# Kernel tuning notes

Measured on AMD Instinct MI355X. Metric: run time of the kernel, lower is better.

The kernel has to match this reference:

```python
import jax, jax.numpy as jnp
import numpy as np

B, S, E, H = 2, 2048, 1024, 16
HD = E // H  # 64
NEG = -1e24


def setup_inputs() -> dict:
    key = jax.random.key(0)
    ks = jax.random.split(key, 20)
    sc_e = 1.0 / np.sqrt(E)
    inp = {
        "q_matrix": jax.random.normal(ks[0], (B, S, E), jnp.float32),
        "k_matrix": jax.random.normal(ks[1], (B, S, E), jnp.float32),
        "v_matrix": jax.random.normal(ks[2], (B, S, E), jnp.float32),
        "mask": jax.random.randint(ks[3], (B, S, S), 0, 2).astype(bool),
        # global QKV projections (embed_dim -> embed_dim)
        "Wq": jax.random.normal(ks[4], (E, E), jnp.float32) * sc_e,
        "bq": jnp.zeros((E,), jnp.float32),
        "Wk": jax.random.normal(ks[5], (E, E), jnp.float32) * sc_e,
        "bk": jnp.zeros((E,), jnp.float32),
        "Wv": jax.random.normal(ks[6], (E, E), jnp.float32) * sc_e,
        "bv": jnp.zeros((E,), jnp.float32),
        # per-head QKV projections (embed_dim -> head_dim), batched over heads
        "Whq": jax.random.normal(ks[7], (H, E, HD), jnp.float32) * sc_e,
        "bhq": jnp.zeros((H, HD), jnp.float32),
        "Whk": jax.random.normal(ks[8], (H, E, HD), jnp.float32) * sc_e,
        "bhk": jnp.zeros((H, HD), jnp.float32),
        "Whv": jax.random.normal(ks[9], (H, E, HD), jnp.float32) * sc_e,
        "bhv": jnp.zeros((H, HD), jnp.float32),
        # output projection
        "Wo": jax.random.normal(ks[10], (E, E), jnp.float32) * sc_e,
        "bo": jnp.zeros((E,), jnp.float32),
    }
    return inp


def reference(q_matrix, k_matrix, v_matrix, mask, Wq, bq, Wk, bk, Wv, bv,
              Whq, bhq, Whk, bhk, Whv, bhv, Wo, bo):
    # global projections [B,S,E]
    qg = q_matrix @ Wq + bq
    kg = k_matrix @ Wk + bk
    vg = v_matrix @ Wv + bv
    # per-head projections -> [B,H,S,HD]
    qh = jnp.einsum('bse,hed->bhsd', qg, Whq) + bhq[None, :, None, :]
    kh = jnp.einsum('bse,hed->bhsd', kg, Whk) + bhk[None, :, None, :]
    vh = jnp.einsum('bse,hed->bhsd', vg, Whv) + bhv[None, :, None, :]
    # scaled dot-product attention, scores [B,H,S,S]
    scores = jnp.einsum('bhsd,bhtd->bhst', qh, kh) / jnp.sqrt(jnp.float32(HD))
    scores = jnp.where(mask[:, None, :, :], NEG, scores)
    weights = jax.nn.softmax(scores, axis=-1)
    out = jnp.einsum('bhst,bhtd->bhsd', weights, vh)
    # concat heads (head order along last dim, matching torch.cat)
    x = out.transpose(0, 2, 1, 3).reshape(out.shape[0], out.shape[2], E)
    return x @ Wo + bo
```

## Files before the change

### kernel.cpp

```cpp
#include <hip/hip_runtime.h>
#include <hip/hip_bf16.h>

typedef unsigned short us16;
typedef __attribute__((ext_vector_type(8))) short short8;
typedef __attribute__((ext_vector_type(4))) float float4v;

#define E_DIM 1024
#define S_LEN 2048
#define B_DIM 2
#define H_DIM 16
#define HD_DIM 64
#define M_ROWS 4096
#define SCALE2 0.18033688011112042f

__device__ __forceinline__ float b2f(us16 b) {
    return __uint_as_float(((unsigned int)b) << 16);
}
__device__ __forceinline__ us16 f2b(float f) {
    unsigned int u = __float_as_uint(f);
    unsigned int r = (u + 0x7fffu + ((u >> 16) & 1u)) >> 16;
    return (us16)r;
}
__device__ __forceinline__ unsigned pack2(float a, float b) {
    return ((__float_as_uint(a) + 0x8000u) >> 16) |
           ((__float_as_uint(b) + 0x8000u) & 0xFFFF0000u);
}

__device__ __forceinline__ void gload16(const us16* g, us16* lds_uniform_base) {
    __builtin_amdgcn_global_load_lds(
        (const __attribute__((address_space(1))) void*)g,
        (__attribute__((address_space(3))) void*)lds_uniform_base, 16, 0, 0);
}

__global__ __launch_bounds__(256) void prep(
    const float* __restrict__ q, const float* __restrict__ k, const float* __restrict__ v,
    const float* __restrict__ Wq, const float* __restrict__ Wk, const float* __restrict__ Wv,
    const float* __restrict__ Whq, const float* __restrict__ Whk, const float* __restrict__ Whv,
    const float* __restrict__ Wo,
    const float* __restrict__ bq, const float* __restrict__ bk, const float* __restrict__ bv,
    const float* __restrict__ bhq, const float* __restrict__ bhk, const float* __restrict__ bhv,
    const int* __restrict__ mask,
    us16* qb, us16* kb, us16* vb, us16* Wqb, us16* Wkb, us16* Wvb,
    us16* WhqT, us16* WhkT, us16* WhvT, us16* WoT,
    unsigned long long* mbits,
    float* bcq, float* bck, float* bcv, float* zbias)
{
    __shared__ us16 tile[32][33];
    __shared__ float red[4][64];
    int blk = blockIdx.x, tid = threadIdx.x;

    if (blk < 7680) {
        const float* in; us16* out; int idx;
        if (blk < 6144) {
            int z = blk >> 11, rem = blk & 2047;
            in = z == 0 ? q : z == 1 ? k : v;
            out = z == 0 ? qb : z == 1 ? kb : vb;
            idx = (rem * 256 + tid) * 8;
        } else {
            int t = blk - 6144, z = t >> 9, rem = t & 511;
            in = z == 0 ? Wq : z == 1 ? Wk : Wv;
            out = z == 0 ? Wqb : z == 1 ? Wkb : Wvb;
            idx = (rem * 256 + tid) * 8;
        }
        float4 f0 = *(const float4*)(in + idx);
        float4 f1 = *(const float4*)(in + idx + 4);
        us16 t8[8] = {f2b(f0.x), f2b(f0.y), f2b(f0.z), f2b(f0.w),
                      f2b(f1.x), f2b(f1.y), f2b(f1.z), f2b(f1.w)};
        *(uint4*)(out + idx) = *(const uint4*)t8;
    } else if (blk < 11776) {
        int t = blk - 7680, z = t >> 10, rem = t & 1023;
        const float* in = z == 0 ? Whq : z == 1 ? Whk : z == 2 ? Whv : Wo;
        us16* out = z == 0 ? WhqT : z == 1 ? WhkT : z == 2 ? WhvT : WoT;
        int mode = (z < 3) ? 1 : 0;
        int bx = rem & 31, by = rem >> 5;
        int tx = tid & 31, ty = tid >> 5;
#pragma unroll
        for (int i = 0; i < 4; ++i) {
            int e = by * 32 + ty + i * 8;
            int c = bx * 32 + tx;
            size_t src;
            if (mode == 0) src = (size_t)e * E_DIM + c;
            else           src = ((size_t)(c >> 6) * E_DIM + e) * 64 + (c & 63);
            tile[ty + i * 8][tx] = f2b(in[src]);
        }
        __syncthreads();
#pragma unroll
        for (int i = 0; i < 4; ++i) {
            int c = bx * 32 + ty + i * 8;
            int e = by * 32 + tx;
            out[(size_t)c * E_DIM + e] = tile[tx][ty + i * 8];
        }
    } else if (blk < 12800) {
        int row = (blk - 11776) * 4 + (tid >> 6);
        int lane = tid & 63;
        const int* mp = mask + (size_t)row * S_LEN;
        for (int w = 0; w < 32; ++w) {
            int mv = mp[w * 64 + lane];
            unsigned long long bal = __ballot(mv != 0);
            if (lane == 0) mbits[(size_t)row * 32 + w] = bal;
        }
    } else if (blk < 12848) {
        int t = blk - 12800, z = t >> 4, h = t & 15;
        const float* bg = z == 0 ? bq : z == 1 ? bk : bv;
        const float* Wh = z == 0 ? Whq : z == 1 ? Whk : Whv;
        const float* bh = z == 0 ? bhq : z == 1 ? bhk : bhv;
        float* bc = z == 0 ? bcq : z == 1 ? bck : bcv;
        float sc = (z == 0) ? SCALE2 : 1.0f;
        int d = tid & 63, part = tid >> 6;
        float acc = 0.f;
        int j0 = part * 256;
        for (int j = j0; j < j0 + 256; ++j)
            acc += bg[j] * Wh[((size_t)h * E_DIM + j) * HD_DIM + d];
        red[part][d] = acc;
        __syncthreads();
        if (tid < 64)
            bc[h * 64 + tid] = (red[0][tid] + red[1][tid] + red[2][tid] + red[3][tid] + bh[h * 64 + tid]) * sc;
    } else {
        int i = (blk - 12848) * 256 + tid;
        if (i < 1024) zbias[i] = 0.f;
    }
}

#define BK 32

__device__ __forceinline__ void gemm_body(
    const us16* __restrict__ A, const us16* __restrict__ Bt,
    const float* __restrict__ bias, void* __restrict__ Cp,
    int M, int N, int K, int bxt, int byt, int omode)
{
    __shared__ us16 As[128 * BK];
    __shared__ us16 Bs[128 * BK];

    int tid = threadIdx.x;
    int wave = tid >> 6, lane = tid & 63;
    int quad = lane >> 4, l16 = lane & 15;
    int wm = (wave >> 1) * 64, wn = (wave & 1) * 64;
    int bm0 = byt * 128, bn0 = bxt * 128;
    int srow = lane >> 2;
    int gcol = (((lane & 3) ^ (srow & 3)) << 3);
    int rslot = ((quad ^ (l16 & 3)) << 3);

    float4v acc[4][4];
#pragma unroll
    for (int i = 0; i < 4; ++i)
#pragma unroll
        for (int j = 0; j < 4; ++j)
#pragma unroll
            for (int r = 0; r < 4; ++r) acc[i][j][r] = 0.f;

    for (int k0 = 0; k0 < K; k0 += BK) {
#pragma unroll
        for (int c = 0; c < 2; ++c) {
            int r0 = 32 * wave + 16 * c;
            gload16(A  + (size_t)(bm0 + r0 + srow) * K + k0 + gcol, &As[r0 * BK]);
            gload16(Bt + (size_t)(bn0 + r0 + srow) * K + k0 + gcol, &Bs[r0 * BK]);
        }
        __syncthreads();
        short8 af[4], bfr[4];
#pragma unroll
        for (int i = 0; i < 4; ++i)
            af[i] = *(const short8*)&As[(wm + i * 16 + l16) * BK + rslot];
#pragma unroll
        for (int j = 0; j < 4; ++j)
            bfr[j] = *(const short8*)&Bs[(wn + j * 16 + l16) * BK + rslot];
#pragma unroll
        for (int i = 0; i < 4; ++i)
#pragma unroll
            for (int j = 0; j < 4; ++j)
                acc[i][j] = __builtin_amdgcn_mfma_f32_16x16x32_bf16(af[i], bfr[j], acc[i][j], 0, 0, 0);
        __syncthreads();
    }

#pragma unroll
    for (int i = 0; i < 4; ++i) {
#pragma unroll
        for (int j = 0; j < 4; ++j) {
#pragma unroll
            for (int r = 0; r < 4; ++r) {
                int row = bm0 + wm + i * 16 + quad * 4 + r;
                int col = bn0 + wn + j * 16 + l16;
                float vv = acc[i][j][r] + ((omode == 3) ? bias[row] : bias[col]);
                if (omode == 1) {
                    int b = row >> 11, s = row & 2047, h = col >> 6, d = col & 63;
                    ((us16*)Cp)[(((size_t)(b * H_DIM + h) * S_LEN + s) * HD_DIM) + d] = f2b(vv);
                } else {
                    int h = row >> 6, d = row & 63, b = col >> 11, sl = col & 2047;
                    ((us16*)Cp)[(((size_t)(b * H_DIM + h) * HD_DIM + d) * S_LEN) + sl] = f2b(vv);
                }
            }
        }
    }
}

__global__ __launch_bounds__(256) void proj_all(
    const us16* __restrict__ qb, const us16* __restrict__ kb, const us16* __restrict__ vb,
    const us16* __restrict__ WcqT, const us16* __restrict__ WckT, const us16* __restrict__ WcvT,
    const float* __restrict__ bcq, const float* __restrict__ bck, const float* __restrict__ bcv,
    us16* __restrict__ qhb, us16* __restrict__ khb, us16* __restrict__ vtb)
{
    int bx = blockIdx.x;
    int z = bx >> 8, t = bx & 255;
    if (z == 0)      gemm_body(qb, WcqT, bcq, qhb, M_ROWS, E_DIM, E_DIM, t & 7, t >> 3, 1);
    else if (z == 1) gemm_body(kb, WckT, bck, khb, M_ROWS, E_DIM, E_DIM, t & 7, t >> 3, 1);
    else             gemm_body(WcvT, vb, bcv, vtb, E_DIM, M_ROWS, E_DIM, t & 31, t >> 5, 3);
}

template<int OMODE>
__device__ __forceinline__ void gemm64_body(
    const us16* __restrict__ A, const us16* __restrict__ Bt,
    const float* __restrict__ bias, void* __restrict__ Cp,
    int M, int N, int K, int bxt, int byt, float oscale)
{
    __shared__ us16 As[64 * BK];
    __shared__ us16 Bs[128 * BK];

    int tid = threadIdx.x;
    int wave = tid >> 6, lane = tid & 63;
    int quad = lane >> 4, l16 = lane & 15;
    int wm = (wave >> 1) * 32, wn = (wave & 1) * 64;
    int bm0 = byt * 64, bn0 = bxt * 128;
    int srow = lane >> 2;
    int gcol = (((lane & 3) ^ (srow & 3)) << 3);
    int rslot = ((quad ^ (l16 & 3)) << 3);

    float4v acc[2][4];
#pragma unroll
    for (int i = 0; i < 2; ++i)
#pragma unroll
        for (int j = 0; j < 4; ++j)
#pragma unroll
            for (int r = 0; r < 4; ++r) acc[i][j][r] = 0.f;

    for (int k0 = 0; k0 < K; k0 += BK) {
        gload16(A + (size_t)(bm0 + 16 * wave + srow) * K + k0 + gcol, &As[16 * wave * BK]);
#pragma unroll
        for (int c = 0; c < 2; ++c) {
            int r0 = 32 * wave + 16 * c;
            gload16(Bt + (size_t)(bn0 + r0 + srow) * K + k0 + gcol, &Bs[r0 * BK]);
        }
        __syncthreads();
        short8 af[2], bfr[4];
#pragma unroll
        for (int i = 0; i < 2; ++i)
            af[i] = *(const short8*)&As[(wm + i * 16 + l16) * BK + rslot];
#pragma unroll
        for (int j = 0; j < 4; ++j)
            bfr[j] = *(const short8*)&Bs[(wn + j * 16 + l16) * BK + rslot];
#pragma unroll
        for (int i = 0; i < 2; ++i)
#pragma unroll
            for (int j = 0; j < 4; ++j)
                acc[i][j] = __builtin_amdgcn_mfma_f32_16x16x32_bf16(af[i], bfr[j], acc[i][j], 0, 0, 0);
        __syncthreads();
    }

#pragma unroll
    for (int i = 0; i < 2; ++i)
#pragma unroll
        for (int j = 0; j < 4; ++j)
#pragma unroll
            for (int r = 0; r < 4; ++r) {
                int row = bm0 + wm + i * 16 + quad * 4 + r;
                int col = bn0 + wn + j * 16 + l16;
                float vv = (acc[i][j][r] + bias[col]) * oscale;
                if (OMODE == 0) ((us16*)Cp)[(size_t)row * N + col] = f2b(vv);
                else            ((float*)Cp)[(size_t)row * N + col] = vv;
            }
}

__global__ __launch_bounds__(256) void wgemm3(
    const us16* A0, const us16* A1, const us16* A2,
    const us16* B0, const us16* B1, const us16* B2,
    const float* zbias, us16* C0, us16* C1, us16* C2)
{
    int z = blockIdx.z;
    const us16* A = z == 0 ? A0 : z == 1 ? A1 : A2;
    const us16* Bt = z == 0 ? B0 : z == 1 ? B1 : B2;
    us16* C = z == 0 ? C0 : z == 1 ? C1 : C2;
    float sc = (z == 0) ? SCALE2 : 1.0f;
    gemm64_body<0>(A, Bt, zbias, C, E_DIM, E_DIM, E_DIM, blockIdx.x, blockIdx.y, sc);
}

__global__ __launch_bounds__(256) void gemm_out64(
    const us16* __restrict__ A, const us16* __restrict__ Bt,
    const float* __restrict__ bias, float* __restrict__ C, int M, int N, int K)
{
    gemm64_body<2>(A, Bt, bias, C, M, N, K, blockIdx.x, blockIdx.y, 1.0f);
}

#define PST 72
#define NT 16

__global__ __launch_bounds__(512) void attn_kernel(
    const us16* __restrict__ qh, const us16* __restrict__ kh,
    const us16* __restrict__ vt, const unsigned long long* __restrict__ mbits,
    us16* __restrict__ o_p, float* __restrict__ l_p)
{
    __shared__ us16 Ks[2][64 * 64];
    __shared__ us16 Vs[2][64 * 64];
    __shared__ us16 Pw[8][16 * PST];

    int tid = threadIdx.x;
    int w = tid >> 6, lane = tid & 63;
    int quad = lane >> 4, l16 = lane & 15;

    int wg = blockIdx.x;
    int xcd = wg & 7, idx = wg >> 3;
    int bh = xcd * 4 + (idx >> 5);
    int rem = idx & 31;
    int z = rem >> 4;
    int q0 = (rem & 15) * 128;
    int b = bh >> 4;
    const size_t base = (size_t)bh * (S_LEN * HD_DIM);

    int qrow = q0 + w * 16 + l16;
    short8 qf0, qf1;
    {
        const us16* qp = qh + base + (size_t)qrow * HD_DIM + quad * 8;
        qf0 = *(const short8*)qp;
        qf1 = *(const short8*)(qp + 32);
    }

    int strow = w * 8 + (lane >> 3);
    int scol = ((lane & 7) ^ (strow & 7)) * 8;
    const us16* ksrc0 = kh + base + ((size_t)(z * 1024 + strow)) * HD_DIM + scol;
    const us16* vsrc0 = vt + base + (size_t)strow * S_LEN + scol + z * 1024;

    int slotA = (quad ^ (l16 & 7)) * 8;
    int slotB = slotA ^ 32;

    float lsum = 0.f;
    float4v o[4];
#pragma unroll
    for (int dt = 0; dt < 4; ++dt)
#pragma unroll
        for (int r = 0; r < 4; ++r) o[dt][r] = 0.f;

    const unsigned long long* mrow = mbits + ((size_t)(b * S_LEN + qrow) * 32) + z * 16;

    gload16(ksrc0, &Ks[0][w * 512]);
    gload16(vsrc0, &Vs[0][w * 512]);
    unsigned long long mw = mrow[0];
    asm volatile("s_waitcnt vmcnt(0)" ::: "memory");
    __builtin_amdgcn_s_barrier();
    __builtin_amdgcn_sched_barrier(0);

    for (int t = 0; t < NT; ++t) {
        int cur = t & 1;
        const us16* KsC = Ks[cur];
        const us16* VsC = Vs[cur];

        unsigned long long mwn = 0ull;
        if (t + 1 < NT) {
            gload16(ksrc0 + (size_t)((t + 1) * 64) * HD_DIM, &Ks[cur ^ 1][w * 512]);
            gload16(vsrc0 + (t + 1) * 64, &Vs[cur ^ 1][w * 512]);
            mwn = mrow[t + 1];
        }

        float4v sc[4];
        __builtin_amdgcn_s_setprio(1);
#pragma unroll
        for (int ct = 0; ct < 4; ++ct) {
            int tt = ct * 16 + l16;
            short8 kf0 = *(const short8*)&KsC[tt * 64 + slotA];
            short8 kf1 = *(const short8*)&KsC[tt * 64 + slotB];
            float4v a;
#pragma unroll
            for (int r = 0; r < 4; ++r) a[r] = 0.f;
            a = __builtin_amdgcn_mfma_f32_16x16x32_bf16(kf0, qf0, a, 0, 0, 0);
            a = __builtin_amdgcn_mfma_f32_16x16x32_bf16(kf1, qf1, a, 0, 0, 0);
            sc[ct] = a;
        }
        __builtin_amdgcn_s_setprio(0);

#pragma unroll
        for (int ct = 0; ct < 4; ++ct) {
            unsigned bits = (unsigned)(mw >> (ct * 16 + quad * 4));
            float p[4];
#pragma unroll
            for (int r = 0; r < 4; ++r) {
                float pin = ((bits >> r) & 1u) ? -1e38f : sc[ct][r];
                p[r] = __builtin_amdgcn_exp2f(pin);
                lsum += p[r];
            }
            uint2 pk;
            pk.x = pack2(p[0], p[1]);
            pk.y = pack2(p[2], p[3]);
            *(uint2*)&Pw[w][l16 * PST + ct * 16 + quad * 4] = pk;
        }

        short8 pf0 = *(const short8*)&Pw[w][l16 * PST + quad * 8];
        short8 pf1 = *(const short8*)&Pw[w][l16 * PST + 32 + quad * 8];
        __builtin_amdgcn_s_setprio(1);
#pragma unroll
        for (int dt = 0; dt < 4; ++dt) {
            int d = dt * 16 + l16;
            short8 vf0 = *(const short8*)&VsC[d * 64 + slotA];
            short8 vf1 = *(const short8*)&VsC[d * 64 + slotB];
            o[dt] = __builtin_amdgcn_mfma_f32_16x16x32_bf16(pf0, vf0, o[dt], 0, 0, 0);
            o[dt] = __builtin_amdgcn_mfma_f32_16x16x32_bf16(pf1, vf1, o[dt], 0, 0, 0);
        }
        __builtin_amdgcn_s_setprio(0);

        mw = mwn;
        asm volatile("s_waitcnt vmcnt(0)" ::: "memory");
        __builtin_amdgcn_s_barrier();
        __builtin_amdgcn_sched_barrier(0);
    }

    lsum += __shfl_xor(lsum, 16, 64);
    lsum += __shfl_xor(lsum, 32, 64);
    if (lane < 16)
        l_p[(size_t)z * 65536 + bh * S_LEN + qrow] = lsum;

    int rowg = bh * S_LEN + q0 + w * 16 + quad * 4;
#pragma unroll
    for (int dt = 0; dt < 4; ++dt)
#pragma unroll
        for (int r = 0; r < 4; ++r)
            o_p[(size_t)z * 4194304 + (size_t)(rowg + r) * 64 + dt * 16 + l16] = f2b(o[dt][r]);
}

__global__ __launch_bounds__(256) void attn_combine(
    const us16* __restrict__ o_p, const float* __restrict__ l_p,
    us16* __restrict__ x)
{
    int fidx = blockIdx.x * 256 + threadIdx.x;
    int rix = fidx >> 3;
    int d8 = (fidx & 7) * 8;
    float linv = 1.0f / (l_p[rix] + l_p[65536 + rix]);
    uint4 a = *(const uint4*)(o_p + (size_t)rix * 64 + d8);
    uint4 c = *(const uint4*)(o_p + 4194304 + (size_t)rix * 64 + d8);
    const us16* ap = (const us16*)&a;
    const us16* cp = (const us16*)&c;
    us16 t8[8];
#pragma unroll
    for (int i = 0; i < 8; ++i)
        t8[i] = f2b((b2f(ap[i]) + b2f(cp[i])) * linv);
    int bh = rix >> 11, b = bh >> 4, h = bh & 15, s = rix & 2047;
    *(uint4*)&x[(size_t)(b * S_LEN + s) * E_DIM + h * HD_DIM + d8] = *(const uint4*)t8;
}

extern "C" void kernel_launch(void* const* d_in, const int* in_sizes, int n_in,
                              void* d_out, int out_size, void* d_ws, size_t ws_size,
                              hipStream_t stream) {
    const float* q    = (const float*)d_in[0];
    const float* k    = (const float*)d_in[1];
    const float* v    = (const float*)d_in[2];
    const int*   mask = (const int*)d_in[3];
    const float* Wq = (const float*)d_in[4];   const float* bq = (const float*)d_in[5];
    const float* Wk = (const float*)d_in[6];   const float* bk = (const float*)d_in[7];
    const float* Wv = (const float*)d_in[8];   const float* bv = (const float*)d_in[9];
    const float* Whq = (const float*)d_in[10]; const float* bhq = (const float*)d_in[11];
    const float* Whk = (const float*)d_in[12]; const float* bhk = (const float*)d_in[13];
    const float* Whv = (const float*)d_in[14]; const float* bhv = (const float*)d_in[15];
    const float* Wo = (const float*)d_in[16];  const float* bo = (const float*)d_in[17];

    us16* ws = (us16*)d_ws;
    const size_t M1 = (size_t)1 << 20;
    us16* WhqT = ws + 0 * M1;
    us16* WhkT = ws + 1 * M1;
    us16* WhvT = ws + 2 * M1;
    us16* WoT  = ws + 3 * M1;
    us16* WcqT = ws + 4 * M1;
    us16* WckT = ws + 5 * M1;
    us16* WcvT = ws + 6 * M1;
    us16* Wqb  = ws + 7 * M1;
    us16* Wkb  = ws + 8 * M1;
    us16* Wvb  = ws + 9 * M1;
    us16* qb   = ws + 10 * M1;
    us16* kb   = ws + 14 * M1;
    us16* vb   = ws + 18 * M1;
    us16* qhb  = ws + 22 * M1;
    us16* khb  = ws + 26 * M1;
    us16* vtb  = ws + 30 * M1;
    us16* o_p  = qb;
    us16* xb   = vb;
    float* bcq   = (float*)(ws + 34 * M1);
    float* bck   = bcq + 1024;
    float* bcv   = bck + 1024;
    float* zbias = bcv + 1024;
    unsigned long long* mbits = (unsigned long long*)(ws + 34 * M1 + 16384);
    float* l_p = (float*)(ws + 34 * M1 + 16384 + 524288);

    prep<<<12852, 256, 0, stream>>>(q, k, v, Wq, Wk, Wv, Whq, Whk, Whv, Wo,
                                    bq, bk, bv, bhq, bhk, bhv, mask,
                                    qb, kb, vb, Wqb, Wkb, Wvb,
                                    WhqT, WhkT, WhvT, WoT, mbits,
                                    bcq, bck, bcv, zbias);

    wgemm3<<<dim3(8, 16, 3), 256, 0, stream>>>(WhqT, WhkT, WhvT, Wqb, Wkb, Wvb, zbias,
                                               WcqT, WckT, WcvT);

    proj_all<<<768, 256, 0, stream>>>(qb, kb, vb, WcqT, WckT, WcvT,
                                      bcq, bck, bcv, qhb, khb, vtb);

    attn_kernel<<<1024, 512, 0, stream>>>(qhb, khb, vtb, mbits, o_p, l_p);
    attn_combine<<<2048, 256, 0, stream>>>(o_p, l_p, xb);

    gemm_out64<<<dim3(8, 64), 256, 0, stream>>>(xb, WoT, bo, (float*)d_out,
                                                M_ROWS, E_DIM, E_DIM);
}
```

Measured before the change: 319.9 us.

## Fold mask into MFMA accumulator init and compute row sums via ones-MFMA

```diff
diff --git a/kernel.cpp b/kernel.cpp
--- a/kernel.cpp
+++ b/kernel.cpp
@@ -20,10 +20,6 @@
     unsigned int u = __float_as_uint(f);
     unsigned int r = (u + 0x7fffu + ((u >> 16) & 1u)) >> 16;
     return (us16)r;
-}
-__device__ __forceinline__ unsigned pack2(float a, float b) {
-    return ((__float_as_uint(a) + 0x8000u) >> 16) |
-           ((__float_as_uint(b) + 0x8000u) & 0xFFFF0000u);
 }
 
 __device__ __forceinline__ void gload16(const us16* g, us16* lds_uniform_base) {
@@ -42,7 +38,7 @@
     const int* __restrict__ mask,
     us16* qb, us16* kb, us16* vb, us16* Wqb, us16* Wkb, us16* Wvb,
     us16* WhqT, us16* WhkT, us16* WhvT, us16* WoT,
-    unsigned long long* mbits,
+    us16* marr,
     float* bcq, float* bck, float* bcv, float* zbias)
 {
     __shared__ us16 tile[32][33];
@@ -90,17 +86,25 @@
             int e = by * 32 + tx;
             out[(size_t)c * E_DIM + e] = tile[tx][ty + i * 8];
         }
-    } else if (blk < 12800) {
-        int row = (blk - 11776) * 4 + (tid >> 6);
-        int lane = tid & 63;
-        const int* mp = mask + (size_t)row * S_LEN;
-        for (int w = 0; w < 32; ++w) {
-            int mv = mp[w * 64 + lane];
-            unsigned long long bal = __ballot(mv != 0);
-            if (lane == 0) mbits[(size_t)row * 32 + w] = bal;
-        }
-    } else if (blk < 12848) {
-        int t = blk - 12800, z = t >> 4, h = t & 15;
+    } else if (blk < 15872) {
+        int g = (blk - 11776) * 256 + tid;
+        int lane = g & 63, ld = (g >> 6) & 1, wv = (g >> 7) & 7;
+        int q0t = (g >> 10) & 15, ktz = (g >> 14) & 31, bb = g >> 19;
+        int quad = lane >> 4, l16 = lane & 15;
+        int qq = q0t * 128 + wv * 16 + l16;
+        int t0 = ktz * 64 + ld * 32 + quad * 4;
+        const int* mp = mask + ((size_t)bb * S_LEN + qq) * S_LEN + t0;
+        int4 ma = *(const int4*)mp;
+        int4 mb2 = *(const int4*)(mp + 16);
+        const us16 NEGB = f2b(-1e38f);
+        us16 t8[8];
+        t8[0] = ma.x ? NEGB : (us16)0;  t8[1] = ma.y ? NEGB : (us16)0;
+        t8[2] = ma.z ? NEGB : (us16)0;  t8[3] = ma.w ? NEGB : (us16)0;
+        t8[4] = mb2.x ? NEGB : (us16)0; t8[5] = mb2.y ? NEGB : (us16)0;
+        t8[6] = mb2.z ? NEGB : (us16)0; t8[7] = mb2.w ? NEGB : (us16)0;
+        *(uint4*)&marr[(size_t)g * 8] = *(const uint4*)t8;
+    } else if (blk < 15920) {
+        int t = blk - 15872, z = t >> 4, h = t & 15;
         const float* bg = z == 0 ? bq : z == 1 ? bk : bv;
         const float* Wh = z == 0 ? Whq : z == 1 ? Whk : Whv;
         const float* bh = z == 0 ? bhq : z == 1 ? bhk : bhv;
@@ -116,7 +120,7 @@
         if (tid < 64)
             bc[h * 64 + tid] = (red[0][tid] + red[1][tid] + red[2][tid] + red[3][tid] + bh[h * 64 + tid]) * sc;
     } else {
-        int i = (blk - 12848) * 256 + tid;
+        int i = (blk - 15920) * 256 + tid;
         if (i < 1024) zbias[i] = 0.f;
     }
 }
@@ -293,7 +297,7 @@
 
 __global__ __launch_bounds__(512) void attn_kernel(
     const us16* __restrict__ qh, const us16* __restrict__ kh,
-    const us16* __restrict__ vt, const unsigned long long* __restrict__ mbits,
+    const us16* __restrict__ vt, const us16* __restrict__ marr,
     us16* __restrict__ o_p, float* __restrict__ l_p)
 {
     __shared__ us16 Ks[2][64 * 64];
@@ -309,7 +313,8 @@
     int bh = xcd * 4 + (idx >> 5);
     int rem = idx & 31;
     int z = rem >> 4;
-    int q0 = (rem & 15) * 128;
+    int q0t = rem & 15;
+    int q0 = q0t * 128;
     int b = bh >> 4;
     const size_t base = (size_t)bh * (S_LEN * HD_DIM);
 
@@ -321,26 +326,34 @@
         qf1 = *(const short8*)(qp + 32);
     }
 
+    short8 onesf;
+#pragma unroll
+    for (int j = 0; j < 8; ++j) onesf[j] = (short)0x3F80;
+
     int strow = w * 8 + (lane >> 3);
     int scol = ((lane & 7) ^ (strow & 7)) * 8;
     const us16* ksrc0 = kh + base + ((size_t)(z * 1024 + strow)) * HD_DIM + scol;
     const us16* vsrc0 = vt + base + (size_t)strow * S_LEN + scol + z * 1024;
 
+    const us16* mb0p = marr + ((((size_t)(b * 32 + z * 16) * 16 + q0t) * 8 + w) * 1024)
+                            + (size_t)lane * 8;
+
     int slotA = (quad ^ (l16 & 7)) * 8;
     int slotB = slotA ^ 32;
 
-    float lsum = 0.f;
     float4v o[4];
 #pragma unroll
     for (int dt = 0; dt < 4; ++dt)
 #pragma unroll
         for (int r = 0; r < 4; ++r) o[dt][r] = 0.f;
-
-    const unsigned long long* mrow = mbits + ((size_t)(b * S_LEN + qrow) * 32) + z * 16;
+    float4v o_l;
+#pragma unroll
+    for (int r = 0; r < 4; ++r) o_l[r] = 0.f;
 
     gload16(ksrc0, &Ks[0][w * 512]);
     gload16(vsrc0, &Vs[0][w * 512]);
-    unsigned long long mw = mrow[0];
+    uint4 mc0 = *(const uint4*)(mb0p);
+    uint4 mc1 = *(const uint4*)(mb0p + 512);
     asm volatile("s_waitcnt vmcnt(0)" ::: "memory");
     __builtin_amdgcn_s_barrier();
     __builtin_amdgcn_sched_barrier(0);
@@ -350,11 +363,13 @@
         const us16* KsC = Ks[cur];
         const us16* VsC = Vs[cur];
 
-        unsigned long long mwn = 0ull;
+        uint4 mn0 = mc0, mn1 = mc1;
         if (t + 1 < NT) {
             gload16(ksrc0 + (size_t)((t + 1) * 64) * HD_DIM, &Ks[cur ^ 1][w * 512]);
             gload16(vsrc0 + (t + 1) * 64, &Vs[cur ^ 1][w * 512]);
-            mwn = mrow[t + 1];
+            const us16* mp = mb0p + (size_t)(t + 1) * 131072;
+            mn0 = *(const uint4*)(mp);
+            mn1 = *(const uint4*)(mp + 512);
         }
 
         float4v sc[4];
@@ -364,9 +379,16 @@
             int tt = ct * 16 + l16;
             short8 kf0 = *(const short8*)&KsC[tt * 64 + slotA];
             short8 kf1 = *(const short8*)&KsC[tt * 64 + slotB];
+            unsigned w0, w1;
+            if (ct == 0)      { w0 = mc0.x; w1 = mc0.y; }
+            else if (ct == 1) { w0 = mc0.z; w1 = mc0.w; }
+            else if (ct == 2) { w0 = mc1.x; w1 = mc1.y; }
+            else              { w0 = mc1.z; w1 = mc1.w; }
             float4v a;
-#pragma unroll
-            for (int r = 0; r < 4; ++r) a[r] = 0.f;
+            a[0] = __uint_as_float(w0 << 16);
+            a[1] = __uint_as_float(w0 & 0xFFFF0000u);
+            a[2] = __uint_as_float(w1 << 16);
+            a[3] = __uint_as_float(w1 & 0xFFFF0000u);
             a = __builtin_amdgcn_mfma_f32_16x16x32_bf16(kf0, qf0, a, 0, 0, 0);
             a = __builtin_amdgcn_mfma_f32_16x16x32_bf16(kf1, qf1, a, 0, 0, 0);
             sc[ct] = a;
@@ -375,17 +397,13 @@
 
 #pragma unroll
         for (int ct = 0; ct < 4; ++ct) {
-            unsigned bits = (unsigned)(mw >> (ct * 16 + quad * 4));
-            float p[4];
-#pragma unroll
-            for (int r = 0; r < 4; ++r) {
-                float pin = ((bits >> r) & 1u) ? -1e38f : sc[ct][r];
-                p[r] = __builtin_amdgcn_exp2f(pin);
-                lsum += p[r];
-            }
+            float p0 = __builtin_amdgcn_exp2f(sc[ct][0]);
+            float p1 = __builtin_amdgcn_exp2f(sc[ct][1]);
+            float p2 = __builtin_amdgcn_exp2f(sc[ct][2]);
+            float p3 = __builtin_amdgcn_exp2f(sc[ct][3]);
             uint2 pk;
-            pk.x = pack2(p[0], p[1]);
-            pk.y = pack2(p[2], p[3]);
+            asm("v_cvt_pk_bf16_f32 %0, %1, %2" : "=v"(pk.x) : "v"(p0), "v"(p1));
+            asm("v_cvt_pk_bf16_f32 %0, %1, %2" : "=v"(pk.y) : "v"(p2), "v"(p3));
             *(uint2*)&Pw[w][l16 * PST + ct * 16 + quad * 4] = pk;
         }
 
@@ -400,18 +418,21 @@
             o[dt] = __builtin_amdgcn_mfma_f32_16x16x32_bf16(pf0, vf0, o[dt], 0, 0, 0);
             o[dt] = __builtin_amdgcn_mfma_f32_16x16x32_bf16(pf1, vf1, o[dt], 0, 0, 0);
         }
+        o_l = __builtin_amdgcn_mfma_f32_16x16x32_bf16(pf0, onesf, o_l, 0, 0, 0);
+        o_l = __builtin_amdgcn_mfma_f32_16x16x32_bf16(pf1, onesf, o_l, 0, 0, 0);
         __builtin_amdgcn_s_setprio(0);
 
-        mw = mwn;
+        mc0 = mn0; mc1 = mn1;
         asm volatile("s_waitcnt vmcnt(0)" ::: "memory");
         __builtin_amdgcn_s_barrier();
         __builtin_amdgcn_sched_barrier(0);
     }
 
-    lsum += __shfl_xor(lsum, 16, 64);
-    lsum += __shfl_xor(lsum, 32, 64);
-    if (lane < 16)
-        l_p[(size_t)z * 65536 + bh * S_LEN + qrow] = lsum;
+    if (l16 == 0) {
+#pragma unroll
+        for (int r = 0; r < 4; ++r)
+            l_p[(size_t)z * 65536 + bh * S_LEN + q0 + w * 16 + quad * 4 + r] = o_l[r];
+    }
 
     int rowg = bh * S_LEN + q0 + w * 16 + quad * 4;
 #pragma unroll
@@ -480,13 +501,13 @@
     float* bck   = bcq + 1024;
     float* bcv   = bck + 1024;
     float* zbias = bcv + 1024;
-    unsigned long long* mbits = (unsigned long long*)(ws + 34 * M1 + 16384);
-    float* l_p = (float*)(ws + 34 * M1 + 16384 + 524288);
-
-    prep<<<12852, 256, 0, stream>>>(q, k, v, Wq, Wk, Wv, Whq, Whk, Whv, Wo,
+    float* l_p   = (float*)(ws + 34 * M1 + 8192);
+    us16*  marr  = ws + 35 * M1;
+
+    prep<<<15924, 256, 0, stream>>>(q, k, v, Wq, Wk, Wv, Whq, Whk, Whv, Wo,
                                     bq, bk, bv, bhq, bhk, bhv, mask,
                                     qb, kb, vb, Wqb, Wkb, Wvb,
-                                    WhqT, WhkT, WhvT, WoT, mbits,
+                                    WhqT, WhkT, WhvT, WoT, marr,
                                     bcq, bck, bcv, zbias);
 
     wgemm3<<<dim3(8, 16, 3), 256, 0, stream>>>(WhqT, WhkT, WhvT, Wqb, Wkb, Wvb, zbias,
@@ -495,7 +516,7 @@
     proj_all<<<768, 256, 0, stream>>>(qb, kb, vb, WcqT, WckT, WcvT,
                                       bcq, bck, bcv, qhb, khb, vtb);
 
-    attn_kernel<<<1024, 512, 0, stream>>>(qhb, khb, vtb, mbits, o_p, l_p);
+    attn_kernel<<<1024, 512, 0, stream>>>(qhb, khb, vtb, marr, o_p, l_p);
     attn_combine<<<2048, 256, 0, stream>>>(o_p, l_p, xb);
 
     gemm_out64<<<dim3(8, 64), 256, 0, stream>>>(xb, WoT, bo, (float*)d_out,
```

Result: faster. 309.2 us (-3.3%).

## Switch attention to 32x32 MFMA with register-resident P and additive bf16 mask

Applied to the files above, without the earlier changes.

```diff
diff --git a/kernel.cpp b/kernel.cpp
--- a/kernel.cpp
+++ b/kernel.cpp
@@ -4,6 +4,8 @@
 typedef unsigned short us16;
 typedef __attribute__((ext_vector_type(8))) short short8;
 typedef __attribute__((ext_vector_type(4))) float float4v;
+typedef __attribute__((ext_vector_type(16))) float float16v;
+typedef __attribute__((ext_vector_type(4))) unsigned uintx4;
 
 #define E_DIM 1024
 #define S_LEN 2048
@@ -20,10 +22,6 @@
     unsigned int u = __float_as_uint(f);
     unsigned int r = (u + 0x7fffu + ((u >> 16) & 1u)) >> 16;
     return (us16)r;
-}
-__device__ __forceinline__ unsigned pack2(float a, float b) {
-    return ((__float_as_uint(a) + 0x8000u) >> 16) |
-           ((__float_as_uint(b) + 0x8000u) & 0xFFFF0000u);
 }
 
 __device__ __forceinline__ void gload16(const us16* g, us16* lds_uniform_base) {
@@ -42,7 +40,7 @@
     const int* __restrict__ mask,
     us16* qb, us16* kb, us16* vb, us16* Wqb, us16* Wkb, us16* Wvb,
     us16* WhqT, us16* WhkT, us16* WhvT, us16* WoT,
-    unsigned long long* mbits,
+    us16* marr,
     float* bcq, float* bck, float* bcv, float* zbias)
 {
     __shared__ us16 tile[32][33];
@@ -90,17 +88,28 @@
             int e = by * 32 + tx;
             out[(size_t)c * E_DIM + e] = tile[tx][ty + i * 8];
         }
-    } else if (blk < 12800) {
-        int row = (blk - 11776) * 4 + (tid >> 6);
-        int lane = tid & 63;
-        const int* mp = mask + (size_t)row * S_LEN;
-        for (int w = 0; w < 32; ++w) {
-            int mv = mp[w * 64 + lane];
-            unsigned long long bal = __ballot(mv != 0);
-            if (lane == 0) mbits[(size_t)row * 32 + w] = bal;
-        }
-    } else if (blk < 12848) {
-        int t = blk - 12800, z = t >> 4, h = t & 15;
+    } else if (blk < 13824) {
+        int g = (blk - 11776) * 256 + tid;
+        int lane = g & 63, tt = (g >> 6) & 1, wv = (g >> 7) & 3;
+        int q0t = (g >> 9) & 15, kt = (g >> 13) & 31, bb = (g >> 18) & 1;
+        int half = lane >> 5;
+        int qq = q0t * 128 + wv * 32 + (lane & 31);
+        int tb = kt * 64 + tt * 32 + 4 * half;
+        const int* mp = mask + ((size_t)bb * S_LEN + qq) * S_LEN + tb;
+        const us16 NEGB = f2b(-1e38f);
+        us16 t16[16];
+#pragma unroll
+        for (int gi = 0; gi < 4; ++gi) {
+            int4 mv = *(const int4*)(mp + gi * 8);
+            t16[gi * 4 + 0] = mv.x ? NEGB : (us16)0;
+            t16[gi * 4 + 1] = mv.y ? NEGB : (us16)0;
+            t16[gi * 4 + 2] = mv.z ? NEGB : (us16)0;
+            t16[gi * 4 + 3] = mv.w ? NEGB : (us16)0;
+        }
+        *(uint4*)&marr[(size_t)g * 16]     = *(const uint4*)&t16[0];
+        *(uint4*)&marr[(size_t)g * 16 + 8] = *(const uint4*)&t16[8];
+    } else if (blk < 13872) {
+        int t = blk - 13824, z = t >> 4, h = t & 15;
         const float* bg = z == 0 ? bq : z == 1 ? bk : bv;
         const float* Wh = z == 0 ? Whq : z == 1 ? Whk : Whv;
         const float* bh = z == 0 ? bhq : z == 1 ? bhk : bhv;
@@ -116,7 +125,7 @@
         if (tid < 64)
             bc[h * 64 + tid] = (red[0][tid] + red[1][tid] + red[2][tid] + red[3][tid] + bh[h * 64 + tid]) * sc;
     } else {
-        int i = (blk - 12848) * 256 + tid;
+        int i = (blk - 13872) * 256 + tid;
         if (i < 1024) zbias[i] = 0.f;
     }
 }
@@ -288,59 +297,93 @@
     gemm64_body<2>(A, Bt, bias, C, M, N, K, blockIdx.x, blockIdx.y, 1.0f);
 }
 
-#define PST 72
 #define NT 16
 
-__global__ __launch_bounds__(512) void attn_kernel(
+__device__ __forceinline__ float16v mask16(uint4 a, uint4 b) {
+    float16v m;
+    unsigned ws[8] = {a.x, a.y, a.z, a.w, b.x, b.y, b.z, b.w};
+#pragma unroll
+    for (int j = 0; j < 8; ++j) {
+        m[2 * j]     = __uint_as_float(ws[j] << 16);
+        m[2 * j + 1] = __uint_as_float(ws[j] & 0xFFFF0000u);
+    }
+    return m;
+}
+
+__device__ __forceinline__ void pfrag(const float16v s, float& lsum,
+                                      short8& flo, short8& fhi) {
+    float p[16];
+#pragma unroll
+    for (int r = 0; r < 16; ++r) p[r] = __builtin_amdgcn_exp2f(s[r]);
+#pragma unroll
+    for (int r = 0; r < 16; ++r) lsum += p[r];
+    unsigned w0, w1, w2, w3, w4, w5, w6, w7;
+    asm("v_cvt_pk_bf16_f32 %0, %1, %2" : "=v"(w0) : "v"(p[0]),  "v"(p[1]));
+    asm("v_cvt_pk_bf16_f32 %0, %1, %2" : "=v"(w1) : "v"(p[2]),  "v"(p[3]));
+    asm("v_cvt_pk_bf16_f32 %0, %1, %2" : "=v"(w2) : "v"(p[4]),  "v"(p[5]));
+    asm("v_cvt_pk_bf16_f32 %0, %1, %2" : "=v"(w3) : "v"(p[6]),  "v"(p[7]));
+    asm("v_cvt_pk_bf16_f32 %0, %1, %2" : "=v"(w4) : "v"(p[8]),  "v"(p[9]));
+    asm("v_cvt_pk_bf16_f32 %0, %1, %2" : "=v"(w5) : "v"(p[10]), "v"(p[11]));
+    asm("v_cvt_pk_bf16_f32 %0, %1, %2" : "=v"(w6) : "v"(p[12]), "v"(p[13]));
+    asm("v_cvt_pk_bf16_f32 %0, %1, %2" : "=v"(w7) : "v"(p[14]), "v"(p[15]));
+    asm("v_permlane32_swap_b32 %0, %1" : "+v"(w0), "+v"(w2));
+    asm("v_permlane32_swap_b32 %0, %1" : "+v"(w1), "+v"(w3));
+    asm("v_permlane32_swap_b32 %0, %1" : "+v"(w4), "+v"(w6));
+    asm("v_permlane32_swap_b32 %0, %1" : "+v"(w5), "+v"(w7));
+    uintx4 lo = {w0, w1, w2, w3}, hi = {w4, w5, w6, w7};
+    flo = __builtin_bit_cast(short8, lo);
+    fhi = __builtin_bit_cast(short8, hi);
+}
+
+__global__ __launch_bounds__(256) void attn_kernel(
     const us16* __restrict__ qh, const us16* __restrict__ kh,
-    const us16* __restrict__ vt, const unsigned long long* __restrict__ mbits,
+    const us16* __restrict__ vt, const us16* __restrict__ marr,
     us16* __restrict__ o_p, float* __restrict__ l_p)
 {
     __shared__ us16 Ks[2][64 * 64];
     __shared__ us16 Vs[2][64 * 64];
-    __shared__ us16 Pw[8][16 * PST];
 
     int tid = threadIdx.x;
     int w = tid >> 6, lane = tid & 63;
-    int quad = lane >> 4, l16 = lane & 15;
+    int q32 = lane & 31, half = lane >> 5;
 
     int wg = blockIdx.x;
     int xcd = wg & 7, idx = wg >> 3;
     int bh = xcd * 4 + (idx >> 5);
     int rem = idx & 31;
     int z = rem >> 4;
-    int q0 = (rem & 15) * 128;
+    int q0t = rem & 15;
+    int q0 = q0t * 128;
     int b = bh >> 4;
     const size_t base = (size_t)bh * (S_LEN * HD_DIM);
 
-    int qrow = q0 + w * 16 + l16;
-    short8 qf0, qf1;
-    {
-        const us16* qp = qh + base + (size_t)qrow * HD_DIM + quad * 8;
-        qf0 = *(const short8*)qp;
-        qf1 = *(const short8*)(qp + 32);
-    }
-
-    int strow = w * 8 + (lane >> 3);
+    int qrow = q0 + w * 32 + q32;
+    short8 qf[4];
+#pragma unroll
+    for (int win = 0; win < 4; ++win)
+        qf[win] = *(const short8*)(qh + base + (size_t)qrow * HD_DIM + win * 16 + half * 8);
+
+    int strow = w * 16 + (lane >> 3);
     int scol = ((lane & 7) ^ (strow & 7)) * 8;
-    const us16* ksrc0 = kh + base + ((size_t)(z * 1024 + strow)) * HD_DIM + scol;
+    const us16* ksrc0 = kh + base + (size_t)(z * 1024 + strow) * HD_DIM + scol;
     const us16* vsrc0 = vt + base + (size_t)strow * S_LEN + scol + z * 1024;
 
-    int slotA = (quad ^ (l16 & 7)) * 8;
-    int slotB = slotA ^ 32;
-
+    const us16* mrec = marr + ((((size_t)(b * 32 + z * 16) * 16 + q0t) * 4 + w) * 2048)
+                            + (size_t)lane * 16;
+
+    float16v oc0, oc1;
+#pragma unroll
+    for (int r = 0; r < 16; ++r) { oc0[r] = 0.f; oc1[r] = 0.f; }
     float lsum = 0.f;
-    float4v o[4];
-#pragma unroll
-    for (int dt = 0; dt < 4; ++dt)
-#pragma unroll
-        for (int r = 0; r < 4; ++r) o[dt][r] = 0.f;
-
-    const unsigned long long* mrow = mbits + ((size_t)(b * S_LEN + qrow) * 32) + z * 16;
-
-    gload16(ksrc0, &Ks[0][w * 512]);
-    gload16(vsrc0, &Vs[0][w * 512]);
-    unsigned long long mw = mrow[0];
+
+    gload16(ksrc0,              &Ks[0][(w * 16) * 64]);
+    gload16(ksrc0 + 8 * HD_DIM, &Ks[0][(w * 16 + 8) * 64]);
+    gload16(vsrc0,              &Vs[0][(w * 16) * 64]);
+    gload16(vsrc0 + 8 * S_LEN,  &Vs[0][(w * 16 + 8) * 64]);
+    uint4 mc0 = *(const uint4*)(mrec);
+    uint4 mc1 = *(const uint4*)(mrec + 8);
+    uint4 mc2 = *(const uint4*)(mrec + 1024);
+    uint4 mc3 = *(const uint4*)(mrec + 1032);
     asm volatile("s_waitcnt vmcnt(0)" ::: "memory");
     __builtin_amdgcn_s_barrier();
     __builtin_amdgcn_sched_barrier(0);
@@ -350,75 +393,84 @@
         const us16* KsC = Ks[cur];
         const us16* VsC = Vs[cur];
 
-        unsigned long long mwn = 0ull;
+        uint4 mn0 = mc0, mn1 = mc1, mn2 = mc2, mn3 = mc3;
         if (t + 1 < NT) {
-            gload16(ksrc0 + (size_t)((t + 1) * 64) * HD_DIM, &Ks[cur ^ 1][w * 512]);
-            gload16(vsrc0 + (t + 1) * 64, &Vs[cur ^ 1][w * 512]);
-            mwn = mrow[t + 1];
-        }
-
-        float4v sc[4];
+            const us16* kn = ksrc0 + (size_t)((t + 1) * 64) * HD_DIM;
+            const us16* vn = vsrc0 + (t + 1) * 64;
+            us16* kd = &Ks[cur ^ 1][(w * 16) * 64];
+            us16* vd = &Vs[cur ^ 1][(w * 16) * 64];
+            gload16(kn,              kd);
+            gload16(kn + 8 * HD_DIM, kd + 8 * 64);
+            gload16(vn,              vd);
+            gload16(vn + 8 * S_LEN,  vd + 8 * 64);
+            const us16* mp = mrec + (size_t)(t + 1) * 131072;
+            mn0 = *(const uint4*)(mp);
+            mn1 = *(const uint4*)(mp + 8);
+            mn2 = *(const uint4*)(mp + 1024);
+            mn3 = *(const uint4*)(mp + 1032);
+        }
+
+        float16v s0 = mask16(mc0, mc1);
+        float16v s1 = mask16(mc2, mc3);
         __builtin_amdgcn_s_setprio(1);
 #pragma unroll
-        for (int ct = 0; ct < 4; ++ct) {
-            int tt = ct * 16 + l16;
-            short8 kf0 = *(const short8*)&KsC[tt * 64 + slotA];
-            short8 kf1 = *(const short8*)&KsC[tt * 64 + slotB];
-            float4v a;
-#pragma unroll
-            for (int r = 0; r < 4; ++r) a[r] = 0.f;
-            a = __builtin_amdgcn_mfma_f32_16x16x32_bf16(kf0, qf0, a, 0, 0, 0);
-            a = __builtin_amdgcn_mfma_f32_16x16x32_bf16(kf1, qf1, a, 0, 0, 0);
-            sc[ct] = a;
+        for (int win = 0; win < 4; ++win) {
+            int sl = ((win * 2 + half) ^ (lane & 7)) * 8;
+            short8 kf0 = *(const short8*)&KsC[q32 * 64 + sl];
+            short8 kf1 = *(const short8*)&KsC[(32 + q32) * 64 + sl];
+            s0 = __builtin_amdgcn_mfma_f32_32x32x16_bf16(kf0, qf[win], s0, 0, 0, 0);
+            s1 = __builtin_amdgcn_mfma_f32_32x32x16_bf16(kf1, qf[win], s1, 0, 0, 0);
         }
         __builtin_amdgcn_s_setprio(0);
 
-#pragma unroll
-        for (int ct = 0; ct < 4; ++ct) {
-            unsigned bits = (unsigned)(mw >> (ct * 16 + quad * 4));
-            float p[4];
-#pragma unroll
-            for (int r = 0; r < 4; ++r) {
-                float pin = ((bits >> r) & 1u) ? -1e38f : sc[ct][r];
-                p[r] = __builtin_amdgcn_exp2f(pin);
-                lsum += p[r];
-            }
-            uint2 pk;
-            pk.x = pack2(p[0], p[1]);
-            pk.y = pack2(p[2], p[3]);
-            *(uint2*)&Pw[w][l16 * PST + ct * 16 + quad * 4] = pk;
-        }
-
-        short8 pf0 = *(const short8*)&Pw[w][l16 * PST + quad * 8];
-        short8 pf1 = *(const short8*)&Pw[w][l16 * PST + 32 + quad * 8];
+        short8 pf0, pf1, pf2, pf3;
+        pfrag(s0, lsum, pf0, pf1);
+        pfrag(s1, lsum, pf2, pf3);
+
         __builtin_amdgcn_s_setprio(1);
-#pragma unroll
-        for (int dt = 0; dt < 4; ++dt) {
-            int d = dt * 16 + l16;
-            short8 vf0 = *(const short8*)&VsC[d * 64 + slotA];
-            short8 vf1 = *(const short8*)&VsC[d * 64 + slotB];
-            o[dt] = __builtin_amdgcn_mfma_f32_16x16x32_bf16(pf0, vf0, o[dt], 0, 0, 0);
-            o[dt] = __builtin_amdgcn_mfma_f32_16x16x32_bf16(pf1, vf1, o[dt], 0, 0, 0);
+        {
+            int sl0 = ((0 * 2 + half) ^ (lane & 7)) * 8;
+            int sl1 = ((1 * 2 + half) ^ (lane & 7)) * 8;
+            int sl2 = ((2 * 2 + half) ^ (lane & 7)) * 8;
+            int sl3 = ((3 * 2 + half) ^ (lane & 7)) * 8;
+            short8 vf;
+            vf = *(const short8*)&VsC[q32 * 64 + sl0];
+            oc0 = __builtin_amdgcn_mfma_f32_32x32x16_bf16(pf0, vf, oc0, 0, 0, 0);
+            vf = *(const short8*)&VsC[(32 + q32) * 64 + sl0];
+            oc1 = __builtin_amdgcn_mfma_f32_32x32x16_bf16(pf0, vf, oc1, 0, 0, 0);
+            vf = *(const short8*)&VsC[q32 * 64 + sl1];
+            oc0 = __builtin_amdgcn_mfma_f32_32x32x16_bf16(pf1, vf, oc0, 0, 0, 0);
+            vf = *(const short8*)&VsC[(32 + q32) * 64 + sl1];
+            oc1 = __builtin_amdgcn_mfma_f32_32x32x16_bf16(pf1, vf, oc1, 0, 0, 0);
+            vf = *(const short8*)&VsC[q32 * 64 + sl2];
+            oc0 = __builtin_amdgcn_mfma_f32_32x32x16_bf16(pf2, vf, oc0, 0, 0, 0);
+            vf = *(const short8*)&VsC[(32 + q32) * 64 + sl2];
+            oc1 = __builtin_amdgcn_mfma_f32_32x32x16_bf16(pf2, vf, oc1, 0, 0, 0);
+            vf = *(const short8*)&VsC[q32 * 64 + sl3];
+            oc0 = __builtin_amdgcn_mfma_f32_32x32x16_bf16(pf3, vf, oc0, 0, 0, 0);
+            vf = *(const short8*)&VsC[(32 + q32) * 64 + sl3];
+            oc1 = __builtin_amdgcn_mfma_f32_32x32x16_bf16(pf3, vf, oc1, 0, 0, 0);
         }
         __builtin_amdgcn_s_setprio(0);
 
-        mw = mwn;
+        mc0 = mn0; mc1 = mn1; mc2 = mn2; mc3 = mn3;
         asm volatile("s_waitcnt vmcnt(0)" ::: "memory");
         __builtin_amdgcn_s_barrier();
         __builtin_amdgcn_sched_barrier(0);
     }
 
-    lsum += __shfl_xor(lsum, 16, 64);
     lsum += __shfl_xor(lsum, 32, 64);
-    if (lane < 16)
-        l_p[(size_t)z * 65536 + bh * S_LEN + qrow] = lsum;
-
-    int rowg = bh * S_LEN + q0 + w * 16 + quad * 4;
-#pragma unroll
-    for (int dt = 0; dt < 4; ++dt)
-#pragma unroll
-        for (int r = 0; r < 4; ++r)
-            o_p[(size_t)z * 4194304 + (size_t)(rowg + r) * 64 + dt * 16 + l16] = f2b(o[dt][r]);
+    if (lane < 32)
+        l_p[(size_t)z * 65536 + bh * S_LEN + q0 + w * 32 + lane] = lsum;
+
+    int rowb = bh * S_LEN + q0 + w * 32;
+#pragma unroll
+    for (int r = 0; r < 16; ++r) {
+        int qq = (r & 3) + 8 * (r >> 2) + 4 * half;
+        size_t ro = (size_t)z * 4194304 + (size_t)(rowb + qq) * 64;
+        o_p[ro + q32]      = f2b(oc0[r]);
+        o_p[ro + 32 + q32] = f2b(oc1[r]);
+    }
 }
 
 __global__ __launch_bounds__(256) void attn_combine(
@@ -480,13 +532,13 @@
     float* bck   = bcq + 1024;
     float* bcv   = bck + 1024;
     float* zbias = bcv + 1024;
-    unsigned long long* mbits = (unsigned long long*)(ws + 34 * M1 + 16384);
-    float* l_p = (float*)(ws + 34 * M1 + 16384 + 524288);
-
-    prep<<<12852, 256, 0, stream>>>(q, k, v, Wq, Wk, Wv, Whq, Whk, Whv, Wo,
+    float* l_p   = (float*)(ws + 34 * M1 + 8192);
+    us16*  marr  = ws + 35 * M1;
+
+    prep<<<13873, 256, 0, stream>>>(q, k, v, Wq, Wk, Wv, Whq, Whk, Whv, Wo,
                                     bq, bk, bv, bhq, bhk, bhv, mask,
                                     qb, kb, vb, Wqb, Wkb, Wvb,
-                                    WhqT, WhkT, WhvT, WoT, mbits,
+                                    WhqT, WhkT, WhvT, WoT, marr,
                                     bcq, bck, bcv, zbias);
 
     wgemm3<<<dim3(8, 16, 3), 256, 0, stream>>>(WhqT, WhkT, WhvT, Wqb, Wkb, Wvb, zbias,
@@ -495,7 +547,7 @@
     proj_all<<<768, 256, 0, stream>>>(qb, kb, vb, WcqT, WckT, WcvT,
                                       bcq, bck, bcv, qhb, khb, vtb);
 
-    attn_kernel<<<1024, 512, 0, stream>>>(qhb, khb, vtb, mbits, o_p, l_p);
+    attn_kernel<<<1024, 256, 0, stream>>>(qhb, khb, vtb, marr, o_p, l_p);
     attn_combine<<<2048, 256, 0, stream>>>(o_p, l_p, xb);
 
     gemm_out64<<<dim3(8, 64), 256, 0, stream>>>(xb, WoT, bo, (float*)d_out,
```

New measurement: 318.0 us. About the same (-0.6%).
